# Kernel tuning notes

Measured on AMD Instinct MI355X. Metric: run time of the kernel, lower is better.

## Reference

```python
import jax, jax.numpy as jnp
import numpy as np

N, E = 10000, 160000
IN_C, HID, OUT_C = 128, 128, 64
LAYERS, HEADS = 3, 8
D_HEAD = HID // HEADS


def setup_inputs() -> dict:
    key = jax.random.key(0)
    ks = jax.random.split(key, 12)
    sc = lambda k, shape, fan: (jax.random.normal(k, shape, jnp.float32) / np.float32(np.sqrt(fan)))
    return dict(
        x=jax.random.normal(ks[0], (N, IN_C), jnp.float32),
        edge_index=jax.random.randint(ks[1], (2, E), 0, N, jnp.int32),
        W1=sc(ks[2], (IN_C, HID), IN_C), b1=jnp.zeros((HID,), jnp.float32),
        Wq=sc(ks[3], (LAYERS, HID, HID), HID), bq=jnp.zeros((LAYERS, HID), jnp.float32),
        Wk=sc(ks[4], (LAYERS, HID, HID), HID), bk=jnp.zeros((LAYERS, HID), jnp.float32),
        Wv=sc(ks[5], (LAYERS, HID, HID), HID), bv=jnp.zeros((LAYERS, HID), jnp.float32),
        W2=sc(ks[6], (HID, OUT_C), HID), b2=jnp.zeros((OUT_C,), jnp.float32),
    )


def reference(x, edge_index, W1, b1, Wq, bq, Wk, bk, Wv, bv, W2, b2):
    n = x.shape[0]
    # gcn_norm with self-loops (edge weights = 1)
    loops = jnp.arange(n, dtype=edge_index.dtype)
    src = jnp.concatenate([edge_index[0], loops])  # x_j source nodes
    dst = jnp.concatenate([edge_index[1], loops])  # x_i target nodes (aggregation)
    deg = jax.ops.segment_sum(jnp.ones_like(src, dtype=x.dtype), dst, num_segments=n)
    dinv = jnp.where(deg > 0, jax.lax.rsqrt(deg), jnp.zeros_like(deg))
    norm = dinv[src] * dinv[dst]  # [E+N]

    # dropout layers are identity in eval mode
    h = jax.nn.relu(x @ W1 + b1)
    x_all = h[:, None, :]  # [N, 1, C]

    scale = np.float32(1.0 / np.sqrt(D_HEAD))
    for l in range(LAYERS):
        L = x_all.shape[1]
        # project at node level (linear commutes with gather)
        q = (x_all[:, -1] @ Wq[l] + bq[l])[dst]              # [Et, C], query = last-layer target feats
        k = (x_all @ Wk[l] + bk[l])[src]                     # [Et, L, C], key = source history
        v = (x_all @ Wv[l] + bv[l])[src]                     # [Et, L, C]
        Et = q.shape[0]
        qh = q.reshape(Et, HEADS, D_HEAD)
        kh = k.reshape(Et, L, HEADS, D_HEAD)
        vh = v.reshape(Et, L, HEADS, D_HEAD)
        scores = jnp.einsum('ehd,elhd->ehl', qh, kh) * scale  # attention over history axis L
        attn = jax.nn.softmax(scores, axis=-1)                 # (attn dropout is identity in eval)
        msg = jnp.einsum('ehl,elhd->ehd', attn, vh).reshape(Et, HID)
        agg = jax.ops.segment_sum(norm[:, None] * msg, dst, num_segments=n)
        h_new = jax.nn.relu(agg)
        x_all = jnp.concatenate([x_all, h_new[:, None, :]], axis=1)

    logits = x_all[:, -1] @ W2 + b2
    return jax.nn.log_softmax(logits, axis=1)
```

## Files before the change

kernel.cpp:

```cpp
#include <hip/hip_runtime.h>
#include <hip/hip_fp16.h>
#include <math.h>

#define NN 10000
#define EE 160000
#define HID 128
constexpr int N128 = NN * HID;
constexpr int PSTR = 768;
constexpr int HOFF = 384;

typedef _Float16 f16;
typedef f16 half8 __attribute__((ext_vector_type(8)));
typedef f16 f16x2 __attribute__((ext_vector_type(2)));
typedef float f32x4 __attribute__((ext_vector_type(4)));

#if __has_builtin(__builtin_amdgcn_fdot2)
__device__ inline float fdot2(f16x2 a, f16x2 b, float c) { return __builtin_amdgcn_fdot2(a, b, c, false); }
#else
__device__ inline float fdot2(f16x2 a, f16x2 b, float c) {
    return fmaf((float)a[0], (float)b[0], fmaf((float)a[1], (float)b[1], c));
}
#endif

__global__ __launch_bounds__(256) void cnt_count(const int* __restrict__ dst, int* __restrict__ cnt) {
    int e = blockIdx.x * 256 + threadIdx.x;
    if (e < EE) atomicAdd(&cnt[dst[e]], 1);
}

__global__ __launch_bounds__(256) void scan_rowptr(const int* __restrict__ cnt, int* __restrict__ rowptr,
                                                   float* __restrict__ dinv) {
    __shared__ int part[256];
    const int PER = (NN + 255) / 256;
    int t = threadIdx.x;
    int base = t * PER;
    int sum = 0;
    for (int i = 0; i < PER; ++i) {
        int idx = base + i;
        if (idx < NN) {
            int c = cnt[idx];
            sum += c;
            dinv[idx] = rsqrtf((float)c + 1.0f);
        }
    }
    part[t] = sum;
    __syncthreads();
    for (int ofs = 1; ofs < 256; ofs <<= 1) {
        int v = (t >= ofs) ? part[t - ofs] : 0;
        __syncthreads();
        part[t] += v;
        __syncthreads();
    }
    int run = (t > 0) ? part[t - 1] : 0;
    for (int i = 0; i < PER; ++i) {
        int idx = base + i;
        if (idx <= NN) rowptr[idx] = run;
        if (idx < NN) run += cnt[idx];
    }
}

__global__ __launch_bounds__(256) void scatter_edges(const int* __restrict__ ei,
                                                     const int* __restrict__ rowptr,
                                                     int* __restrict__ fill,
                                                     int* __restrict__ esorted) {
    int e = blockIdx.x * 256 + threadIdx.x;
    if (e < EE) {
        int s = ei[e], d = ei[EE + e];
        int pos = rowptr[d] + atomicAdd(&fill[d], 1);
        esorted[pos] = s;
    }
}

__global__ __launch_bounds__(256) void prep_fused(const float* __restrict__ W1, const float* __restrict__ Wq,
                                                  const float* __restrict__ Wk, const float* __restrict__ Wv,
                                                  const float* __restrict__ W2, f16* __restrict__ Wt,
                                                  int4* __restrict__ zbuf) {
    int b = blockIdx.x;
    int t = threadIdx.x;
    if (b >= 11) {
        zbuf[(b - 11) * 256 + t] = make_int4(0, 0, 0, 0);
        return;
    }
    f16* dst = Wt + (size_t)b * 16384;
    if (b == 10) {
        int oc = t & 63, k0 = (t >> 6) * 32;
        for (int kk = 0; kk < 32; ++kk) {
            int k = k0 + kk;
            dst[oc * 128 + k] = (f16)W2[(size_t)k * 64 + oc];
        }
        return;
    }
    const float* src = (b == 0) ? W1
                     : (b < 4)  ? Wq + (size_t)(b - 1) * 16384
                     : (b < 7)  ? Wk + (size_t)(b - 4) * 16384
                                : Wv + (size_t)(b - 7) * 16384;
    int oc = t >> 1;
    int k0 = (t & 1) * 64;
    for (int kk = 0; kk < 64; ++kk) {
        int k = k0 + kk;
        dst[oc * 128 + k] = (f16)src[k * 128 + oc];
    }
}

struct GJob {
    const void* in; const f16* Wt; const float* bias; const float* rowscale;
    void* out; int ldi; int ldo; int mode; int inF32;
    const f16* Wt2; const float* bias2;
};
struct GJobs { GJob j[7]; };

__global__ __launch_bounds__(256) void gemm_mfma(GJobs jobs, int nrows) {
    const GJob jb = jobs.j[blockIdx.y];
    __shared__ f16 Xl[64 * 128];
    __shared__ f16 Wl[128 * 128];
    const int t = threadIdx.x;
    const int row0 = blockIdx.x * 64;

    half8 zero8;
#pragma unroll
    for (int z = 0; z < 8; ++z) zero8[z] = (f16)0.f;

#pragma unroll
    for (int it = 0; it < 4; ++it) {
        int idx = t + it * 256;
        int r = idx >> 4, c = idx & 15;
        int gr = row0 + r;
        half8 v = zero8;
        if (gr < nrows) {
            if (jb.inF32) {
                const float* fin = (const float*)jb.in + (size_t)gr * jb.ldi + c * 8;
                float4 f0 = ((const float4*)fin)[0];
                float4 f1 = ((const float4*)fin)[1];
                v[0] = (f16)f0.x; v[1] = (f16)f0.y; v[2] = (f16)f0.z; v[3] = (f16)f0.w;
                v[4] = (f16)f1.x; v[5] = (f16)f1.y; v[6] = (f16)f1.z; v[7] = (f16)f1.w;
            } else {
                v = *(const half8*)((const f16*)jb.in + (size_t)gr * jb.ldi + c * 8);
            }
        }
        *(half8*)((char*)Xl + r * 256 + ((c * 16) ^ ((r & 7) << 4))) = v;
    }
#pragma unroll
    for (int it = 0; it < 8; ++it) {
        int idx = t + it * 256;
        int r = idx >> 4, c = idx & 15;
        half8 v = *(const half8*)(jb.Wt + (size_t)r * 128 + c * 8);
        *(half8*)((char*)Wl + r * 256 + ((c * 16) ^ ((r & 7) << 4))) = v;
    }
    __syncthreads();

    const int w = t >> 6, l = t & 63;
    const int lr = l & 15;
    const int lk = l >> 4;

    f32x4 acc[8];
#pragma unroll
    for (int tn = 0; tn < 8; ++tn)
#pragma unroll
        for (int i = 0; i < 4; ++i) acc[tn][i] = 0.f;

    const int arow = w * 16 + lr;
    const int axor = (arow & 7) << 4;
    const int bxor = (lr & 7) << 4;

#pragma unroll
    for (int ks = 0; ks < 4; ++ks) {
        int koff = (ks * 4 + lk) * 16;
        half8 a = *(const half8*)((const char*)Xl + arow * 256 + (koff ^ axor));
#pragma unroll
        for (int tn = 0; tn < 8; ++tn) {
            int oc = tn * 16 + lr;
            half8 b = *(const half8*)((const char*)Wl + oc * 256 + (koff ^ bxor));
            acc[tn] = __builtin_amdgcn_mfma_f32_16x16x32_f16(a, b, acc[tn], 0, 0, 0);
        }
    }

    const int rbase = row0 + w * 16 + (lk << 2);
    float brs[4];
#pragma unroll
    for (int i = 0; i < 4; ++i)
        brs[i] = jb.rowscale ? ((rbase + i < nrows) ? jb.rowscale[rbase + i] : 0.f) : 1.0f;
    float bsv[8];
#pragma unroll
    for (int tn = 0; tn < 8; ++tn) bsv[tn] = jb.bias[tn * 16 + lr];

    if (jb.mode == 0) {
        float* op = (float*)jb.out;
#pragma unroll
        for (int tn = 0; tn < 8; ++tn)
#pragma unroll
            for (int i = 0; i < 4; ++i) {
                int gr = rbase + i;
                if (gr < nrows) op[(size_t)gr * jb.ldo + tn * 16 + lr] = acc[tn][i] + brs[i] * bsv[tn];
            }
    } else if (jb.mode == 1) {
        f16* op = (f16*)jb.out;
#pragma unroll
        for (int tn = 0; tn < 8; ++tn)
#pragma unroll
            for (int i = 0; i < 4; ++i) {
                int gr = rbase + i;
                if (gr < nrows) op[(size_t)gr * jb.ldo + tn * 16 + lr] = (f16)fmaxf(acc[tn][i] + brs[i] * bsv[tn], 0.f);
            }
    } else if (jb.mode == 2) {
        f16* op = (f16*)jb.out;
#pragma unroll
        for (int tn = 0; tn < 8; ++tn)
#pragma unroll
            for (int i = 0; i < 4; ++i) {
                int gr = rbase + i;
                if (gr < nrows) op[(size_t)gr * jb.ldo + tn * 16 + lr] = (f16)(acc[tn][i] + brs[i] * bsv[tn]);
            }
    } else {
        __syncthreads();
#pragma unroll
        for (int tn = 0; tn < 8; ++tn)
#pragma unroll
            for (int i = 0; i < 4; ++i) {
                f16 v = (f16)fmaxf(acc[tn][i] + brs[i] * bsv[tn], 0.f);
                int lrow = w * 16 + (lk << 2) + i;
                int col = tn * 16 + lr;
                int byte = lrow * 256 + ((((col >> 3) * 16) ^ ((lrow & 7) << 4))) + (col & 7) * 2;
                *(f16*)((char*)Xl + byte) = v;
            }
#pragma unroll
        for (int it = 0; it < 4; ++it) {
            int idx = t + it * 256;
            int r = idx >> 4, c = idx & 15;
            half8 v = *(const half8*)(jb.Wt2 + (size_t)r * 128 + c * 8);
            *(half8*)((char*)Wl + r * 256 + ((c * 16) ^ ((r & 7) << 4))) = v;
        }
        __syncthreads();

        f32x4 acc2[4];
#pragma unroll
        for (int tn = 0; tn < 4; ++tn)
#pragma unroll
            for (int i = 0; i < 4; ++i) acc2[tn][i] = 0.f;
#pragma unroll
        for (int ks = 0; ks < 4; ++ks) {
            int koff = (ks * 4 + lk) * 16;
            half8 a = *(const half8*)((const char*)Xl + arow * 256 + (koff ^ axor));
#pragma unroll
            for (int tn = 0; tn < 4; ++tn) {
                int oc = tn * 16 + lr;
                half8 b = *(const half8*)((const char*)Wl + oc * 256 + (koff ^ bxor));
                acc2[tn] = __builtin_amdgcn_mfma_f32_16x16x32_f16(a, b, acc2[tn], 0, 0, 0);
            }
        }
        float bs2[4];
#pragma unroll
        for (int tn = 0; tn < 4; ++tn) bs2[tn] = jb.bias2[tn * 16 + lr];
#pragma unroll
        for (int i = 0; i < 4; ++i) {
            float lg[4];
#pragma unroll
            for (int tn = 0; tn < 4; ++tn) lg[tn] = acc2[tn][i] + bs2[tn];
            float m = fmaxf(fmaxf(lg[0], lg[1]), fmaxf(lg[2], lg[3]));
#pragma unroll
            for (int sft = 1; sft <= 8; sft <<= 1) m = fmaxf(m, __shfl_xor(m, sft));
            float den = 0.f;
#pragma unroll
            for (int tn = 0; tn < 4; ++tn) den += __expf(lg[tn] - m);
#pragma unroll
            for (int sft = 1; sft <= 8; sft <<= 1) den += __shfl_xor(den, sft);
            float lden = logf(den);
            int gr = rbase + i;
            if (gr < nrows) {
                float* op = (float*)jb.out + (size_t)gr * jb.ldo;
#pragma unroll
                for (int tn = 0; tn < 4; ++tn) op[tn * 16 + lr] = lg[tn] - m - lden;
            }
        }
    }
}

__global__ __launch_bounds__(256) void sgather5(
    const int* __restrict__ rowptr, const int* __restrict__ esorted,
    const float* __restrict__ dinv,
    const f16* __restrict__ hsrc , f16* __restrict__ Sh, float* __restrict__ srow) {
    int d = (blockIdx.x * 256 + threadIdx.x) >> 6;
    int lam = threadIdx.x & 63;
    int qe = lam >> 4, le = lam & 15;
    if (d >= NN) return;
    int i0 = rowptr[d], nE = rowptr[d + 1] - i0 + 1;
    float dvd = dinv[d];
    float u[8];
#pragma unroll
    for (int i = 0; i < 8; ++i) u[i] = 0.f;
    float ssum = 0.f;

    auto ldb = [&](int b, float& w, half8& h) {
        int j = b + qe;
        int s = (j < nE - 1) ? esorted[i0 + j] : d;
        w = (j < nE) ? dinv[s] : 0.f;
        h = *(const half8*)(hsrc + (size_t)s * PSTR + le * 8);
    };
    auto cmp = [&](float w, const half8& h) {
#pragma unroll
        for (int i = 0; i < 8; ++i) u[i] = fmaf(w, (float)h[i], u[i]);
        ssum += w;
    };

    float wA, wB; half8 hA, hB;
    ldb(0, wA, hA);
    for (int b = 0; b < nE; b += 8) {
        ldb(b + 4, wB, hB);
        cmp(wA, hA);
        ldb(b + 8, wA, hA);
        cmp(wB, hB);
    }
#pragma unroll
    for (int i = 0; i < 8; ++i) {
        u[i] += __shfl_xor(u[i], 16);
        u[i] += __shfl_xor(u[i], 32);
    }
    ssum += __shfl_xor(ssum, 16);
    ssum += __shfl_xor(ssum, 32);
    if (qe == 0) {
        half8 o;
#pragma unroll
        for (int i = 0; i < 8; ++i) o[i] = (f16)(dvd * u[i]);
        *(half8*)(Sh + (size_t)d * 128 + le * 8) = o;
        if (le == 0) srow[d] = dvd * ssum;
    }
}

template<int L>
__global__ __launch_bounds__(256) void node_attn5(
    const int* __restrict__ rowptr, const int* __restrict__ esorted,
    const float* __restrict__ dinv,
    const f16* __restrict__ qh, const f16* __restrict__ pack,
    f16* __restrict__ uh) {
    int d = (blockIdx.x * 256 + threadIdx.x) >> 6;
    int lam = threadIdx.x & 63;
    int qe = lam >> 4, le = lam & 15;
    if (d >= NN) return;
    int i0 = rowptr[d], nE = rowptr[d + 1] - i0 + 1;
    float dvd = dinv[d];
    half8 q8 = *(const half8*)(qh + (size_t)d * 128 + le * 8);
    const f16x2* qp = (const f16x2*)&q8;
    float u[8];
#pragma unroll
    for (int i = 0; i < 8; ++i) u[i] = 0.f;

    auto ldb = [&](int b, float& w, half8 (&k)[L], half8 (&h)[L]) {
        int j = b + qe;
        int s = (j < nE - 1) ? esorted[i0 + j] : d;
        w = (j < nE) ? dinv[s] : 0.f;
        const f16* bp = pack + (size_t)s * PSTR + le * 8;
#pragma unroll
        for (int l = 0; l < L; ++l) {
            k[l] = *(const half8*)(bp + l * 128);
            h[l] = *(const half8*)(bp + HOFF + l * 128);
        }
    };
    auto cmp = [&](float w, const half8 (&k)[L], const half8 (&h)[L]) {
        float sc[L];
#pragma unroll
        for (int l = 0; l < L; ++l) {
            const f16x2* kp = (const f16x2*)&k[l];
            float p = 0.f;
#pragma unroll
            for (int i = 0; i < 4; ++i) p = fdot2(qp[i], kp[i], p);
            p += __shfl_xor(p, 1);
            sc[l] = p * 0.25f;
        }
        float m = sc[0];
#pragma unroll
        for (int l = 1; l < L; ++l) m = fmaxf(m, sc[l]);
        float den = 0.f;
#pragma unroll
        for (int l = 0; l < L; ++l) { sc[l] = __expf(sc[l] - m); den += sc[l]; }
        float wg = w * __builtin_amdgcn_rcpf(den);
#pragma unroll
        for (int l = 0; l < L; ++l) {
            float a = sc[l] * wg;
#pragma unroll
            for (int i = 0; i < 8; ++i) u[i] = fmaf(a, (float)h[l][i], u[i]);
        }
    };

    float wA, wB; half8 kA[L], hA[L], kB[L], hB[L];
    ldb(0, wA, kA, hA);
    for (int b = 0; b < nE; b += 8) {
        ldb(b + 4, wB, kB, hB);
        cmp(wA, kA, hA);
        ldb(b + 8, wA, kA, hA);
        cmp(wB, kB, hB);
    }
#pragma unroll
    for (int i = 0; i < 8; ++i) {
        u[i] += __shfl_xor(u[i], 16);
        u[i] += __shfl_xor(u[i], 32);
    }
    if (qe == 0) {
        half8 o;
#pragma unroll
        for (int i = 0; i < 8; ++i) o[i] = (f16)(dvd * u[i]);
        *(half8*)(uh + (size_t)d * 128 + le * 8) = o;
    }
}

extern "C" void kernel_launch(void* const* d_in, const int* in_sizes, int n_in,
                              void* d_out, int out_size, void* d_ws, size_t ws_size,
                              hipStream_t stream) {
    (void)in_sizes; (void)n_in; (void)out_size; (void)ws_size;
    const float* x  = (const float*)d_in[0];
    const int*   ei = (const int*)d_in[1];
    const float* W1 = (const float*)d_in[2];
    const float* b1 = (const float*)d_in[3];
    const float* Wq = (const float*)d_in[4];
    const float* bq = (const float*)d_in[5];
    const float* Wk = (const float*)d_in[6];
    const float* bk = (const float*)d_in[7];
    const float* Wv = (const float*)d_in[8];
    const float* bv = (const float*)d_in[9];
    const float* W2 = (const float*)d_in[10];
    const float* b2 = (const float*)d_in[11];
    float* out = (float*)d_out;

    int*    cnt     = (int*)d_ws;
    int*    fill    = cnt + 16384;
    int*    rowptr  = fill + 16384;
    int*    esorted = rowptr + 16384;
    float*  dinv    = (float*)(esorted + 163840);
    float*  srow    = dinv + 16384;
    f16*    pack    = (f16*)(srow + 16384);
    f16*    Sh      = pack + (size_t)NN * PSTR;
    f16*    qh      = Sh + N128;
    f16*    uh      = qh + N128;
    f16*    Wt      = uh + N128;

    prep_fused<<<43, 256, 0, stream>>>(W1, Wq, Wk, Wv, W2, Wt, (int4*)cnt);
    cnt_count<<<(EE + 255) / 256, 256, 0, stream>>>(ei + EE, cnt);
    scan_rowptr<<<1, 256, 0, stream>>>(cnt, rowptr, dinv);
    scatter_edges<<<(EE + 255) / 256, 256, 0, stream>>>(ei, rowptr, fill, esorted);

    const int gx = (NN + 63) / 64;
    auto WT = [&](int m) { return Wt + (size_t)m * 16384; };
    auto H  = [&](int lev) { return pack + HOFF + lev * 128; };
    auto K  = [&](int lev) { return pack + lev * 128; };

    {
        GJobs jobs{};
        jobs.j[0] = {x, WT(0), b1, nullptr, H(0), HID, PSTR, 1, 1, nullptr, nullptr};
        gemm_mfma<<<dim3(gx, 1), 256, 0, stream>>>(jobs, NN);
    }

    const int nblocks = (NN * 64 + 255) / 256;

    sgather5<<<nblocks, 256, 0, stream>>>(rowptr, esorted, dinv, pack + HOFF, Sh, srow);
    {
        GJobs jobs{};
        jobs.j[0] = {Sh, WT(7), bv, srow, H(1), HID, PSTR, 1, 0, nullptr, nullptr};
        gemm_mfma<<<dim3(gx, 1), 256, 0, stream>>>(jobs, NN);
    }

    for (int l = 1; l < 3; ++l) {
        int L = l + 1;
        GJobs jobs{};
        jobs.j[0] = {H(L - 1), WT(1 + l), bq + l * HID, nullptr, qh, PSTR, HID, 2, 0, nullptr, nullptr};
        for (int lev = 0; lev < L; ++lev)
            jobs.j[1 + lev] = {H(lev), WT(4 + l), bk + l * HID, nullptr, K(lev), PSTR, PSTR, 2, 0, nullptr, nullptr};
        gemm_mfma<<<dim3(gx, 1 + L), 256, 0, stream>>>(jobs, NN);

        if (L == 2) node_attn5<2><<<nblocks, 256, 0, stream>>>(rowptr, esorted, dinv, qh, pack, uh);
        if (L == 3) node_attn5<3><<<nblocks, 256, 0, stream>>>(rowptr, esorted, dinv, qh, pack, uh);

        GJobs vjob{};
        if (L == 2) {
            vjob.j[0] = {uh, WT(7 + l), bv + l * HID, srow, H(2), HID, PSTR, 1, 0, nullptr, nullptr};
        } else {
            vjob.j[0] = {uh, WT(7 + l), bv + l * HID, srow, out, HID, 64, 3, 0, WT(10), b2};
        }
        gemm_mfma<<<dim3(gx, 1), 256, 0, stream>>>(vjob, NN);
    }
}
```

Measured before the change: 169.0 us.

## Fold Wq·Wkᵀ per head so attention scores use stored hidden states

```diff
diff --git a/kernel.cpp b/kernel.cpp
--- a/kernel.cpp
+++ b/kernel.cpp
@@ -6,8 +6,7 @@
 #define EE 160000
 #define HID 128
 constexpr int N128 = NN * HID;
-constexpr int PSTR = 768;
-constexpr int HOFF = 384;
+constexpr int PSTR = 384;
 
 typedef _Float16 f16;
 typedef f16 half8 __attribute__((ext_vector_type(8)));
@@ -70,34 +69,61 @@
     }
 }
 
-__global__ __launch_bounds__(256) void prep_fused(const float* __restrict__ W1, const float* __restrict__ Wq,
-                                                  const float* __restrict__ Wk, const float* __restrict__ Wv,
-                                                  const float* __restrict__ W2, f16* __restrict__ Wt,
-                                                  int4* __restrict__ zbuf) {
+__global__ __launch_bounds__(256) void prep_fused(
+    const float* __restrict__ W1, const float* __restrict__ Wq, const float* __restrict__ Wk,
+    const float* __restrict__ Wv, const float* __restrict__ W2, const float* __restrict__ bq,
+    f16* __restrict__ Wt, f16* __restrict__ Wqkt, float* __restrict__ bqk, int4* __restrict__ zbuf) {
+    __shared__ float Wqs[128][16];
+    __shared__ float Wks[128][16];
     int b = blockIdx.x;
     int t = threadIdx.x;
-    if (b >= 11) {
-        zbuf[(b - 11) * 256 + t] = make_int4(0, 0, 0, 0);
+    if (b >= 21) {
+        zbuf[(b - 21) * 256 + t] = make_int4(0, 0, 0, 0);
         return;
     }
-    f16* dst = Wt + (size_t)b * 16384;
-    if (b == 10) {
-        int oc = t & 63, k0 = (t >> 6) * 32;
-        for (int kk = 0; kk < 32; ++kk) {
+    if (b < 5) {
+        f16* dst = Wt + (size_t)b * 16384;
+        if (b == 4) {
+            int oc = t & 63, k0 = (t >> 6) * 32;
+            for (int kk = 0; kk < 32; ++kk) {
+                int k = k0 + kk;
+                dst[oc * 128 + k] = (f16)W2[(size_t)k * 64 + oc];
+            }
+            return;
+        }
+        const float* src = (b == 0) ? W1 : Wv + (size_t)(b - 1) * 16384;
+        int oc = t >> 1;
+        int k0 = (t & 1) * 64;
+        for (int kk = 0; kk < 64; ++kk) {
             int k = k0 + kk;
-            dst[oc * 128 + k] = (f16)W2[(size_t)k * 64 + oc];
+            dst[oc * 128 + k] = (f16)src[k * 128 + oc];
         }
         return;
     }
-    const float* src = (b == 0) ? W1
-                     : (b < 4)  ? Wq + (size_t)(b - 1) * 16384
-                     : (b < 7)  ? Wk + (size_t)(b - 4) * 16384
-                                : Wv + (size_t)(b - 7) * 16384;
-    int oc = t >> 1;
-    int k0 = (t & 1) * 64;
-    for (int kk = 0; kk < 64; ++kk) {
-        int k = k0 + kk;
-        dst[oc * 128 + k] = (f16)src[k * 128 + oc];
+    int idx = b - 5;
+    int l = 1 + (idx >> 3), h = idx & 7;
+    const float* WqL = Wq + (size_t)l * 16384;
+    const float* WkL = Wk + (size_t)l * 16384;
+    for (int i = t; i < 2048; i += 256) {
+        int r = i >> 4, c = i & 15;
+        Wqs[r][c] = WqL[r * 128 + h * 16 + c];
+        Wks[r][c] = WkL[r * 128 + h * 16 + c];
+    }
+    __syncthreads();
+    f16* dst = Wqkt + (size_t)idx * 16384;
+    int j = t >> 1, i0 = (t & 1) * 64;
+    for (int ii = 0; ii < 64; ++ii) {
+        int i = i0 + ii;
+        float s = 0.f;
+#pragma unroll
+        for (int c = 0; c < 16; ++c) s = fmaf(Wqs[i][c], Wks[j][c], s);
+        dst[j * 128 + i] = (f16)s;
+    }
+    if (t < 128) {
+        float s = 0.f;
+#pragma unroll
+        for (int c = 0; c < 16; ++c) s = fmaf(bq[l * 128 + h * 16 + c], Wks[t][c], s);
+        bqk[idx * 128 + t] = s;
     }
 }
 
@@ -106,7 +132,7 @@
     void* out; int ldi; int ldo; int mode; int inF32;
     const f16* Wt2; const float* bias2;
 };
-struct GJobs { GJob j[7]; };
+struct GJobs { GJob j[8]; };
 
 __global__ __launch_bounds__(256) void gemm_mfma(GJobs jobs, int nrows) {
     const GJob jb = jobs.j[blockIdx.y];
@@ -325,10 +351,10 @@
 }
 
 template<int L>
-__global__ __launch_bounds__(256) void node_attn5(
+__global__ __launch_bounds__(256) void node_attn6(
     const int* __restrict__ rowptr, const int* __restrict__ esorted,
     const float* __restrict__ dinv,
-    const f16* __restrict__ qh, const f16* __restrict__ pack,
+    const f16* __restrict__ qkb, const f16* __restrict__ pack,
     f16* __restrict__ uh) {
     int d = (blockIdx.x * 256 + threadIdx.x) >> 6;
     int lam = threadIdx.x & 63;
@@ -336,56 +362,69 @@
     if (d >= NN) return;
     int i0 = rowptr[d], nE = rowptr[d + 1] - i0 + 1;
     float dvd = dinv[d];
-    half8 q8 = *(const half8*)(qh + (size_t)d * 128 + le * 8);
-    const f16x2* qp = (const f16x2*)&q8;
+    half8 qk8[8];
+#pragma unroll
+    for (int hh = 0; hh < 8; ++hh)
+        qk8[hh] = *(const half8*)(qkb + (size_t)d * 1024 + hh * 128 + le * 8);
+    const int g = le >> 1;
+    const bool b2g = g >= 4, b1g = (g & 2) != 0, b0g = (g & 1) != 0;
     float u[8];
 #pragma unroll
     for (int i = 0; i < 8; ++i) u[i] = 0.f;
 
-    auto ldb = [&](int b, float& w, half8 (&k)[L], half8 (&h)[L]) {
+    auto ldb = [&](int b, float& w, half8 (&h)[L]) {
         int j = b + qe;
         int s = (j < nE - 1) ? esorted[i0 + j] : d;
         w = (j < nE) ? dinv[s] : 0.f;
         const f16* bp = pack + (size_t)s * PSTR + le * 8;
 #pragma unroll
+        for (int l = 0; l < L; ++l) h[l] = *(const half8*)(bp + l * 128);
+    };
+    auto cmp = [&](float w, const half8 (&h)[L]) {
+        float sel[L];
+#pragma unroll
         for (int l = 0; l < L; ++l) {
-            k[l] = *(const half8*)(bp + l * 128);
-            h[l] = *(const half8*)(bp + HOFF + l * 128);
+            float ph[8];
+#pragma unroll
+            for (int hh = 0; hh < 8; ++hh) {
+                const f16x2* ap = (const f16x2*)&qk8[hh];
+                const f16x2* hp = (const f16x2*)&h[l];
+                float p = 0.f;
+#pragma unroll
+                for (int i = 0; i < 4; ++i) p = fdot2(ap[i], hp[i], p);
+                ph[hh] = p;
+            }
+#pragma unroll
+            for (int st = 1; st <= 8; st <<= 1) {
+#pragma unroll
+                for (int hh = 0; hh < 8; ++hh) ph[hh] += __shfl_xor(ph[hh], st);
+            }
+            float a = b2g ? (b1g ? (b0g ? ph[7] : ph[6]) : (b0g ? ph[5] : ph[4]))
+                          : (b1g ? (b0g ? ph[3] : ph[2]) : (b0g ? ph[1] : ph[0]));
+            sel[l] = a * 0.25f;
+        }
+        float m = sel[0];
+#pragma unroll
+        for (int l = 1; l < L; ++l) m = fmaxf(m, sel[l]);
+        float den = 0.f;
+#pragma unroll
+        for (int l = 0; l < L; ++l) { sel[l] = __expf(sel[l] - m); den += sel[l]; }
+        float wg = w * __builtin_amdgcn_rcpf(den);
+#pragma unroll
+        for (int l = 0; l < L; ++l) {
+            float a = sel[l] * wg;
+#pragma unroll
+            for (int i = 0; i < 8; ++i) u[i] = fmaf(a, (float)h[l][i], u[i]);
         }
     };
-    auto cmp = [&](float w, const half8 (&k)[L], const half8 (&h)[L]) {
-        float sc[L];
-#pragma unroll
-        for (int l = 0; l < L; ++l) {
-            const f16x2* kp = (const f16x2*)&k[l];
-            float p = 0.f;
-#pragma unroll
-            for (int i = 0; i < 4; ++i) p = fdot2(qp[i], kp[i], p);
-            p += __shfl_xor(p, 1);
-            sc[l] = p * 0.25f;
-        }
-        float m = sc[0];
-#pragma unroll
-        for (int l = 1; l < L; ++l) m = fmaxf(m, sc[l]);
-        float den = 0.f;
-#pragma unroll
-        for (int l = 0; l < L; ++l) { sc[l] = __expf(sc[l] - m); den += sc[l]; }
-        float wg = w * __builtin_amdgcn_rcpf(den);
-#pragma unroll
-        for (int l = 0; l < L; ++l) {
-            float a = sc[l] * wg;
-#pragma unroll
-            for (int i = 0; i < 8; ++i) u[i] = fmaf(a, (float)h[l][i], u[i]);
-        }
-    };
-
-    float wA, wB; half8 kA[L], hA[L], kB[L], hB[L];
-    ldb(0, wA, kA, hA);
+
+    float wA, wB; half8 hA[L], hB[L];
+    ldb(0, wA, hA);
     for (int b = 0; b < nE; b += 8) {
-        ldb(b + 4, wB, kB, hB);
-        cmp(wA, kA, hA);
-        ldb(b + 8, wA, kA, hA);
-        cmp(wB, kB, hB);
+        ldb(b + 4, wB, hB);
+        cmp(wA, hA);
+        ldb(b + 8, wA, hA);
+        cmp(wB, hB);
     }
 #pragma unroll
     for (int i = 0; i < 8; ++i) {
@@ -417,6 +456,7 @@
     const float* W2 = (const float*)d_in[10];
     const float* b2 = (const float*)d_in[11];
     float* out = (float*)d_out;
+    (void)bk;
 
     int*    cnt     = (int*)d_ws;
     int*    fill    = cnt + 16384;
@@ -424,21 +464,22 @@
     int*    esorted = rowptr + 16384;
     float*  dinv    = (float*)(esorted + 163840);
     float*  srow    = dinv + 16384;
-    f16*    pack    = (f16*)(srow + 16384);
+    float*  bqk     = srow + 16384;
+    f16*    pack    = (f16*)(bqk + 2048);
     f16*    Sh      = pack + (size_t)NN * PSTR;
-    f16*    qh      = Sh + N128;
-    f16*    uh      = qh + N128;
-    f16*    Wt      = uh + N128;
-
-    prep_fused<<<43, 256, 0, stream>>>(W1, Wq, Wk, Wv, W2, Wt, (int4*)cnt);
+    f16*    uh      = Sh + N128;
+    f16*    qkbuf   = uh + N128;
+    f16*    Wt      = qkbuf + (size_t)NN * 1024;
+    f16*    Wqkt    = Wt + 5 * 16384;
+
+    prep_fused<<<53, 256, 0, stream>>>(W1, Wq, Wk, Wv, W2, bq, Wt, Wqkt, bqk, (int4*)cnt);
     cnt_count<<<(EE + 255) / 256, 256, 0, stream>>>(ei + EE, cnt);
     scan_rowptr<<<1, 256, 0, stream>>>(cnt, rowptr, dinv);
     scatter_edges<<<(EE + 255) / 256, 256, 0, stream>>>(ei, rowptr, fill, esorted);
 
     const int gx = (NN + 63) / 64;
     auto WT = [&](int m) { return Wt + (size_t)m * 16384; };
-    auto H  = [&](int lev) { return pack + HOFF + lev * 128; };
-    auto K  = [&](int lev) { return pack + lev * 128; };
+    auto H  = [&](int lev) { return pack + lev * 128; };
 
     {
         GJobs jobs{};
@@ -448,29 +489,31 @@
 
     const int nblocks = (NN * 64 + 255) / 256;
 
-    sgather5<<<nblocks, 256, 0, stream>>>(rowptr, esorted, dinv, pack + HOFF, Sh, srow);
+    sgather5<<<nblocks, 256, 0, stream>>>(rowptr, esorted, dinv, pack, Sh, srow);
     {
         GJobs jobs{};
-        jobs.j[0] = {Sh, WT(7), bv, srow, H(1), HID, PSTR, 1, 0, nullptr, nullptr};
+        jobs.j[0] = {Sh, WT(1), bv, srow, H(1), HID, PSTR, 1, 0, nullptr, nullptr};
         gemm_mfma<<<dim3(gx, 1), 256, 0, stream>>>(jobs, NN);
     }
 
     for (int l = 1; l < 3; ++l) {
         int L = l + 1;
         GJobs jobs{};
-        jobs.j[0] = {H(L - 1), WT(1 + l), bq + l * HID, nullptr, qh, PSTR, HID, 2, 0, nullptr, nullptr};
-        for (int lev = 0; lev < L; ++lev)
-            jobs.j[1 + lev] = {H(lev), WT(4 + l), bk + l * HID, nullptr, K(lev), PSTR, PSTR, 2, 0, nullptr, nullptr};
-        gemm_mfma<<<dim3(gx, 1 + L), 256, 0, stream>>>(jobs, NN);
-
-        if (L == 2) node_attn5<2><<<nblocks, 256, 0, stream>>>(rowptr, esorted, dinv, qh, pack, uh);
-        if (L == 3) node_attn5<3><<<nblocks, 256, 0, stream>>>(rowptr, esorted, dinv, qh, pack, uh);
+        for (int h = 0; h < 8; ++h) {
+            int idx = (l - 1) * 8 + h;
+            jobs.j[h] = {H(L - 1), Wqkt + (size_t)idx * 16384, bqk + idx * 128, nullptr,
+                         qkbuf + h * 128, PSTR, 1024, 2, 0, nullptr, nullptr};
+        }
+        gemm_mfma<<<dim3(gx, 8), 256, 0, stream>>>(jobs, NN);
+
+        if (L == 2) node_attn6<2><<<nblocks, 256, 0, stream>>>(rowptr, esorted, dinv, qkbuf, pack, uh);
+        if (L == 3) node_attn6<3><<<nblocks, 256, 0, stream>>>(rowptr, esorted, dinv, qkbuf, pack, uh);
 
         GJobs vjob{};
         if (L == 2) {
-            vjob.j[0] = {uh, WT(7 + l), bv + l * HID, srow, H(2), HID, PSTR, 1, 0, nullptr, nullptr};
+            vjob.j[0] = {uh, WT(2), bv + 128, srow, H(2), HID, PSTR, 1, 0, nullptr, nullptr};
         } else {
-            vjob.j[0] = {uh, WT(7 + l), bv + l * HID, srow, out, HID, 64, 3, 0, WT(10), b2};
+            vjob.j[0] = {uh, WT(3), bv + 256, srow, out, HID, 64, 3, 0, WT(4), b2};
         }
         gemm_mfma<<<dim3(gx, 1), 256, 0, stream>>>(vjob, NN);
     }
```

Measured after the change: 238.9 us. 41.3% more time.

## Split per-node edge aggregation across two wavefronts with partial-sum buffers

Applied to the files above, without the earlier changes.

```diff
diff --git a/kernel.cpp b/kernel.cpp
--- a/kernel.cpp
+++ b/kernel.cpp
@@ -104,7 +104,7 @@
 struct GJob {
     const void* in; const f16* Wt; const float* bias; const float* rowscale;
     void* out; int ldi; int ldo; int mode; int inF32;
-    const f16* Wt2; const float* bias2;
+    const f16* Wt2; const float* bias2; const f16* in2;
 };
 struct GJobs { GJob j[7]; };
 
@@ -134,6 +134,10 @@
                 v[4] = (f16)f1.x; v[5] = (f16)f1.y; v[6] = (f16)f1.z; v[7] = (f16)f1.w;
             } else {
                 v = *(const half8*)((const f16*)jb.in + (size_t)gr * jb.ldi + c * 8);
+                if (jb.in2) {
+                    half8 v2 = *(const half8*)(jb.in2 + (size_t)gr * jb.ldi + c * 8);
+                    v = v + v2;
+                }
             }
         }
         *(half8*)((char*)Xl + r * 256 + ((c * 16) ^ ((r & 7) << 4))) = v;
@@ -273,15 +277,19 @@
     }
 }
 
-__global__ __launch_bounds__(256) void sgather5(
+__global__ __launch_bounds__(256) void sgather6(
     const int* __restrict__ rowptr, const int* __restrict__ esorted,
     const float* __restrict__ dinv,
-    const f16* __restrict__ hsrc , f16* __restrict__ Sh, float* __restrict__ srow) {
-    int d = (blockIdx.x * 256 + threadIdx.x) >> 6;
+    const f16* __restrict__ hsrc , f16* __restrict__ Sh0, f16* __restrict__ Sh1,
+    float* __restrict__ srow) {
+    int wid = (blockIdx.x * 256 + threadIdx.x) >> 6;
     int lam = threadIdx.x & 63;
     int qe = lam >> 4, le = lam & 15;
-    if (d >= NN) return;
+    if (wid >= 2 * NN) return;
+    int d = wid >> 1, half = wid & 1;
     int i0 = rowptr[d], nE = rowptr[d + 1] - i0 + 1;
+    int mid = (nE + 1) >> 1;
+    int lo = half ? mid : 0, hi = half ? nE : mid;
     float dvd = dinv[d];
     float u[8];
 #pragma unroll
@@ -291,7 +299,7 @@
     auto ldb = [&](int b, float& w, half8& h) {
         int j = b + qe;
         int s = (j < nE - 1) ? esorted[i0 + j] : d;
-        w = (j < nE) ? dinv[s] : 0.f;
+        w = (j < hi) ? dinv[s] : 0.f;
         h = *(const half8*)(hsrc + (size_t)s * PSTR + le * 8);
     };
     auto cmp = [&](float w, const half8& h) {
@@ -301,8 +309,8 @@
     };
 
     float wA, wB; half8 hA, hB;
-    ldb(0, wA, hA);
-    for (int b = 0; b < nE; b += 8) {
+    ldb(lo, wA, hA);
+    for (int b = lo; b < hi; b += 8) {
         ldb(b + 4, wB, hB);
         cmp(wA, hA);
         ldb(b + 8, wA, hA);
@@ -316,25 +324,29 @@
     ssum += __shfl_xor(ssum, 16);
     ssum += __shfl_xor(ssum, 32);
     if (qe == 0) {
+        f16* Sh = half ? Sh1 : Sh0;
         half8 o;
 #pragma unroll
         for (int i = 0; i < 8; ++i) o[i] = (f16)(dvd * u[i]);
         *(half8*)(Sh + (size_t)d * 128 + le * 8) = o;
-        if (le == 0) srow[d] = dvd * ssum;
+        if (le == 0) atomicAdd(&srow[d], dvd * ssum);
     }
 }
 
 template<int L>
-__global__ __launch_bounds__(256) void node_attn5(
+__global__ __launch_bounds__(256) void node_attn7(
     const int* __restrict__ rowptr, const int* __restrict__ esorted,
     const float* __restrict__ dinv,
     const f16* __restrict__ qh, const f16* __restrict__ pack,
-    f16* __restrict__ uh) {
-    int d = (blockIdx.x * 256 + threadIdx.x) >> 6;
+    f16* __restrict__ uh0, f16* __restrict__ uh1) {
+    int wid = (blockIdx.x * 256 + threadIdx.x) >> 6;
     int lam = threadIdx.x & 63;
     int qe = lam >> 4, le = lam & 15;
-    if (d >= NN) return;
+    if (wid >= 2 * NN) return;
+    int d = wid >> 1, half = wid & 1;
     int i0 = rowptr[d], nE = rowptr[d + 1] - i0 + 1;
+    int mid = (nE + 1) >> 1;
+    int lo = half ? mid : 0, hi = half ? nE : mid;
     float dvd = dinv[d];
     half8 q8 = *(const half8*)(qh + (size_t)d * 128 + le * 8);
     const f16x2* qp = (const f16x2*)&q8;
@@ -345,7 +357,7 @@
     auto ldb = [&](int b, float& w, half8 (&k)[L], half8 (&h)[L]) {
         int j = b + qe;
         int s = (j < nE - 1) ? esorted[i0 + j] : d;
-        w = (j < nE) ? dinv[s] : 0.f;
+        w = (j < hi) ? dinv[s] : 0.f;
         const f16* bp = pack + (size_t)s * PSTR + le * 8;
 #pragma unroll
         for (int l = 0; l < L; ++l) {
@@ -380,8 +392,8 @@
     };
 
     float wA, wB; half8 kA[L], hA[L], kB[L], hB[L];
-    ldb(0, wA, kA, hA);
-    for (int b = 0; b < nE; b += 8) {
+    ldb(lo, wA, kA, hA);
+    for (int b = lo; b < hi; b += 8) {
         ldb(b + 4, wB, kB, hB);
         cmp(wA, kA, hA);
         ldb(b + 8, wA, kA, hA);
@@ -393,6 +405,7 @@
         u[i] += __shfl_xor(u[i], 32);
     }
     if (qe == 0) {
+        f16* uh = half ? uh1 : uh0;
         half8 o;
 #pragma unroll
         for (int i = 0; i < 8; ++i) o[i] = (f16)(dvd * u[i]);
@@ -420,17 +433,19 @@
 
     int*    cnt     = (int*)d_ws;
     int*    fill    = cnt + 16384;
-    int*    rowptr  = fill + 16384;
+    float*  srow    = (float*)(fill + 16384);
+    int*    rowptr  = (int*)(srow + 16384);
     int*    esorted = rowptr + 16384;
     float*  dinv    = (float*)(esorted + 163840);
-    float*  srow    = dinv + 16384;
-    f16*    pack    = (f16*)(srow + 16384);
-    f16*    Sh      = pack + (size_t)NN * PSTR;
-    f16*    qh      = Sh + N128;
-    f16*    uh      = qh + N128;
-    f16*    Wt      = uh + N128;
-
-    prep_fused<<<43, 256, 0, stream>>>(W1, Wq, Wk, Wv, W2, Wt, (int4*)cnt);
+    f16*    pack    = (f16*)(dinv + 16384);
+    f16*    Sh0     = pack + (size_t)NN * PSTR;
+    f16*    Sh1     = Sh0 + N128;
+    f16*    qh      = Sh1 + N128;
+    f16*    uh0     = qh + N128;
+    f16*    uh1     = uh0 + N128;
+    f16*    Wt      = uh1 + N128;
+
+    prep_fused<<<59, 256, 0, stream>>>(W1, Wq, Wk, Wv, W2, Wt, (int4*)cnt);
     cnt_count<<<(EE + 255) / 256, 256, 0, stream>>>(ei + EE, cnt);
     scan_rowptr<<<1, 256, 0, stream>>>(cnt, rowptr, dinv);
     scatter_edges<<<(EE + 255) / 256, 256, 0, stream>>>(ei, rowptr, fill, esorted);
@@ -442,35 +457,35 @@
 
     {
         GJobs jobs{};
-        jobs.j[0] = {x, WT(0), b1, nullptr, H(0), HID, PSTR, 1, 1, nullptr, nullptr};
+        jobs.j[0] = {x, WT(0), b1, nullptr, H(0), HID, PSTR, 1, 1, nullptr, nullptr, nullptr};
         gemm_mfma<<<dim3(gx, 1), 256, 0, stream>>>(jobs, NN);
     }
 
-    const int nblocks = (NN * 64 + 255) / 256;
-
-    sgather5<<<nblocks, 256, 0, stream>>>(rowptr, esorted, dinv, pack + HOFF, Sh, srow);
+    const int nblocks = (2 * NN * 64 + 255) / 256;
+
+    sgather6<<<nblocks, 256, 0, stream>>>(rowptr, esorted, dinv, pack + HOFF, Sh0, Sh1, srow);
     {
         GJobs jobs{};
-        jobs.j[0] = {Sh, WT(7), bv, srow, H(1), HID, PSTR, 1, 0, nullptr, nullptr};
+        jobs.j[0] = {Sh0, WT(7), bv, srow, H(1), HID, PSTR, 1, 0, nullptr, nullptr, Sh1};
         gemm_mfma<<<dim3(gx, 1), 256, 0, stream>>>(jobs, NN);
     }
 
     for (int l = 1; l < 3; ++l) {
         int L = l + 1;
         GJobs jobs{};
-        jobs.j[0] = {H(L - 1), WT(1 + l), bq + l * HID, nullptr, qh, PSTR, HID, 2, 0, nullptr, nullptr};
+        jobs.j[0] = {H(L - 1), WT(1 + l), bq + l * HID, nullptr, qh, PSTR, HID, 2, 0, nullptr, nullptr, nullptr};
         for (int lev = 0; lev < L; ++lev)
-            jobs.j[1 + lev] = {H(lev), WT(4 + l), bk + l * HID, nullptr, K(lev), PSTR, PSTR, 2, 0, nullptr, nullptr};
+            jobs.j[1 + lev] = {H(lev), WT(4 + l), bk + l * HID, nullptr, K(lev), PSTR, PSTR, 2, 0, nullptr, nullptr, nullptr};
         gemm_mfma<<<dim3(gx, 1 + L), 256, 0, stream>>>(jobs, NN);
 
-        if (L == 2) node_attn5<2><<<nblocks, 256, 0, stream>>>(rowptr, esorted, dinv, qh, pack, uh);
-        if (L == 3) node_attn5<3><<<nblocks, 256, 0, stream>>>(rowptr, esorted, dinv, qh, pack, uh);
+        if (L == 2) node_attn7<2><<<nblocks, 256, 0, stream>>>(rowptr, esorted, dinv, qh, pack, uh0, uh1);
+        if (L == 3) node_attn7<3><<<nblocks, 256, 0, stream>>>(rowptr, esorted, dinv, qh, pack, uh0, uh1);
 
         GJobs vjob{};
         if (L == 2) {
-            vjob.j[0] = {uh, WT(7 + l), bv + l * HID, srow, H(2), HID, PSTR, 1, 0, nullptr, nullptr};
+            vjob.j[0] = {uh0, WT(7 + l), bv + l * HID, srow, H(2), HID, PSTR, 1, 0, nullptr, nullptr, uh1};
         } else {
-            vjob.j[0] = {uh, WT(7 + l), bv + l * HID, srow, out, HID, 64, 3, 0, WT(10), b2};
+            vjob.j[0] = {uh0, WT(7 + l), bv + l * HID, srow, out, HID, 64, 3, 0, WT(10), b2, uh1};
         }
         gemm_mfma<<<dim3(gx, 1), 256, 0, stream>>>(vjob, NN);
     }
```

New measurement: 178.4 us. +5.6%, slower.

## Chain Q/K projections into the producing GEMM epilogue and drop separate projection launches

Applied to the files above, without the earlier changes.

```diff
diff --git a/kernel.cpp b/kernel.cpp
--- a/kernel.cpp
+++ b/kernel.cpp
@@ -6,8 +6,8 @@
 #define EE 160000
 #define HID 128
 constexpr int N128 = NN * HID;
-constexpr int PSTR = 768;
-constexpr int HOFF = 384;
+constexpr int PST = 1024;
+constexpr int H0 = 640;
 
 typedef _Float16 f16;
 typedef f16 half8 __attribute__((ext_vector_type(8)));
@@ -28,7 +28,7 @@
 }
 
 __global__ __launch_bounds__(256) void scan_rowptr(const int* __restrict__ cnt, int* __restrict__ rowptr,
-                                                   float* __restrict__ dinv) {
+                                                   int* __restrict__ rowfill, float* __restrict__ dinv) {
     __shared__ int part[256];
     const int PER = (NN + 255) / 256;
     int t = threadIdx.x;
@@ -54,18 +54,17 @@
     for (int i = 0; i < PER; ++i) {
         int idx = base + i;
         if (idx <= NN) rowptr[idx] = run;
-        if (idx < NN) run += cnt[idx];
+        if (idx < NN) { rowfill[idx] = run; run += cnt[idx]; }
     }
 }
 
 __global__ __launch_bounds__(256) void scatter_edges(const int* __restrict__ ei,
-                                                     const int* __restrict__ rowptr,
-                                                     int* __restrict__ fill,
+                                                     int* __restrict__ rowfill,
                                                      int* __restrict__ esorted) {
     int e = blockIdx.x * 256 + threadIdx.x;
     if (e < EE) {
         int s = ei[e], d = ei[EE + e];
-        int pos = rowptr[d] + atomicAdd(&fill[d], 1);
+        int pos = atomicAdd(&rowfill[d], 1);
         esorted[pos] = s;
     }
 }
@@ -76,12 +75,12 @@
                                                   int4* __restrict__ zbuf) {
     int b = blockIdx.x;
     int t = threadIdx.x;
-    if (b >= 11) {
-        zbuf[(b - 11) * 256 + t] = make_int4(0, 0, 0, 0);
+    if (b >= 9) {
+        zbuf[(b - 9) * 256 + t] = make_int4(0, 0, 0, 0);
         return;
     }
     f16* dst = Wt + (size_t)b * 16384;
-    if (b == 10) {
+    if (b == 4) {
         int oc = t & 63, k0 = (t >> 6) * 32;
         for (int kk = 0; kk < 32; ++kk) {
             int k = k0 + kk;
@@ -90,9 +89,11 @@
         return;
     }
     const float* src = (b == 0) ? W1
-                     : (b < 4)  ? Wq + (size_t)(b - 1) * 16384
-                     : (b < 7)  ? Wk + (size_t)(b - 4) * 16384
-                                : Wv + (size_t)(b - 7) * 16384;
+                     : (b <= 3) ? Wv + (size_t)(b - 1) * 16384
+                     : (b == 5) ? Wq + 16384
+                     : (b == 6) ? Wq + 2 * 16384
+                     : (b == 7) ? Wk + 16384
+                                : Wk + 2 * 16384;
     int oc = t >> 1;
     int k0 = (t & 1) * 64;
     for (int kk = 0; kk < 64; ++kk) {
@@ -101,15 +102,16 @@
     }
 }
 
-struct GJob {
-    const void* in; const f16* Wt; const float* bias; const float* rowscale;
-    void* out; int ldi; int ldo; int mode; int inF32;
-    const f16* Wt2; const float* bias2;
+struct Proj { const f16* Wt; const float* bias; f16* out; int ldo; };
+struct FJob {
+    const void* in; int inF32; int ldi;
+    const f16* Wt; const float* bias; const float* rowscale;
+    f16* out; int ldo; int writeOut;
+    int nproj; Proj proj[3];
+    int doFinal; const f16* Wt2; const float* bias2; float* fout;
 };
-struct GJobs { GJob j[7]; };
-
-__global__ __launch_bounds__(256) void gemm_mfma(GJobs jobs, int nrows) {
-    const GJob jb = jobs.j[blockIdx.y];
+
+__global__ __launch_bounds__(256) void gemm_fused(FJob jb, int nrows) {
     __shared__ f16 Xl[64 * 128];
     __shared__ f16 Wl[128 * 128];
     const int t = threadIdx.x;
@@ -150,16 +152,15 @@
     const int w = t >> 6, l = t & 63;
     const int lr = l & 15;
     const int lk = l >> 4;
-
-    f32x4 acc[8];
-#pragma unroll
-    for (int tn = 0; tn < 8; ++tn)
-#pragma unroll
-        for (int i = 0; i < 4; ++i) acc[tn][i] = 0.f;
-
     const int arow = w * 16 + lr;
     const int axor = (arow & 7) << 4;
     const int bxor = (lr & 7) << 4;
+
+    f32x4 acc[8];
+#pragma unroll
+    for (int tn = 0; tn < 8; ++tn)
+#pragma unroll
+        for (int i = 0; i < 4; ++i) acc[tn][i] = 0.f;
 
 #pragma unroll
     for (int ks = 0; ks < 4; ++ks) {
@@ -182,45 +183,60 @@
 #pragma unroll
     for (int tn = 0; tn < 8; ++tn) bsv[tn] = jb.bias[tn * 16 + lr];
 
-    if (jb.mode == 0) {
-        float* op = (float*)jb.out;
+#pragma unroll
+    for (int tn = 0; tn < 8; ++tn)
+#pragma unroll
+        for (int i = 0; i < 4; ++i) {
+            f16 v = (f16)fmaxf(acc[tn][i] + brs[i] * bsv[tn], 0.f);
+            int lrow = w * 16 + (lk << 2) + i;
+            int col = tn * 16 + lr;
+            int byte = lrow * 256 + (((col >> 3) * 16) ^ ((lrow & 7) << 4)) + (col & 7) * 2;
+            *(f16*)((char*)Xl + byte) = v;
+            int gr = rbase + i;
+            if (jb.writeOut && gr < nrows) jb.out[(size_t)gr * jb.ldo + col] = v;
+        }
+
+    for (int p = 0; p < jb.nproj; ++p) {
+        Proj pr = jb.proj[p];
+        __syncthreads();
+#pragma unroll
+        for (int it = 0; it < 8; ++it) {
+            int idx = t + it * 256;
+            int r = idx >> 4, c = idx & 15;
+            half8 v = *(const half8*)(pr.Wt + (size_t)r * 128 + c * 8);
+            *(half8*)((char*)Wl + r * 256 + ((c * 16) ^ ((r & 7) << 4))) = v;
+        }
+        __syncthreads();
+
+#pragma unroll
+        for (int tn = 0; tn < 8; ++tn)
+#pragma unroll
+            for (int i = 0; i < 4; ++i) acc[tn][i] = 0.f;
+#pragma unroll
+        for (int ks = 0; ks < 4; ++ks) {
+            int koff = (ks * 4 + lk) * 16;
+            half8 a = *(const half8*)((const char*)Xl + arow * 256 + (koff ^ axor));
+#pragma unroll
+            for (int tn = 0; tn < 8; ++tn) {
+                int oc = tn * 16 + lr;
+                half8 b = *(const half8*)((const char*)Wl + oc * 256 + (koff ^ bxor));
+                acc[tn] = __builtin_amdgcn_mfma_f32_16x16x32_f16(a, b, acc[tn], 0, 0, 0);
+            }
+        }
+        float bp[8];
+#pragma unroll
+        for (int tn = 0; tn < 8; ++tn) bp[tn] = pr.bias[tn * 16 + lr];
 #pragma unroll
         for (int tn = 0; tn < 8; ++tn)
 #pragma unroll
             for (int i = 0; i < 4; ++i) {
                 int gr = rbase + i;
-                if (gr < nrows) op[(size_t)gr * jb.ldo + tn * 16 + lr] = acc[tn][i] + brs[i] * bsv[tn];
+                if (gr < nrows) pr.out[(size_t)gr * pr.ldo + tn * 16 + lr] = (f16)(acc[tn][i] + bp[tn]);
             }
-    } else if (jb.mode == 1) {
-        f16* op = (f16*)jb.out;
-#pragma unroll
-        for (int tn = 0; tn < 8; ++tn)
-#pragma unroll
-            for (int i = 0; i < 4; ++i) {
-                int gr = rbase + i;
-                if (gr < nrows) op[(size_t)gr * jb.ldo + tn * 16 + lr] = (f16)fmaxf(acc[tn][i] + brs[i] * bsv[tn], 0.f);
-            }
-    } else if (jb.mode == 2) {
-        f16* op = (f16*)jb.out;
-#pragma unroll
-        for (int tn = 0; tn < 8; ++tn)
-#pragma unroll
-            for (int i = 0; i < 4; ++i) {
-                int gr = rbase + i;
-                if (gr < nrows) op[(size_t)gr * jb.ldo + tn * 16 + lr] = (f16)(acc[tn][i] + brs[i] * bsv[tn]);
-            }
-    } else {
+    }
+
+    if (jb.doFinal) {
         __syncthreads();
-#pragma unroll
-        for (int tn = 0; tn < 8; ++tn)
-#pragma unroll
-            for (int i = 0; i < 4; ++i) {
-                f16 v = (f16)fmaxf(acc[tn][i] + brs[i] * bsv[tn], 0.f);
-                int lrow = w * 16 + (lk << 2) + i;
-                int col = tn * 16 + lr;
-                int byte = lrow * 256 + ((((col >> 3) * 16) ^ ((lrow & 7) << 4))) + (col & 7) * 2;
-                *(f16*)((char*)Xl + byte) = v;
-            }
 #pragma unroll
         for (int it = 0; it < 4; ++it) {
             int idx = t + it * 256;
@@ -265,7 +281,7 @@
             float lden = logf(den);
             int gr = rbase + i;
             if (gr < nrows) {
-                float* op = (float*)jb.out + (size_t)gr * jb.ldo;
+                float* op = jb.fout + (size_t)gr * 64;
 #pragma unroll
                 for (int tn = 0; tn < 4; ++tn) op[tn * 16 + lr] = lg[tn] - m - lden;
             }
@@ -276,7 +292,7 @@
 __global__ __launch_bounds__(256) void sgather5(
     const int* __restrict__ rowptr, const int* __restrict__ esorted,
     const float* __restrict__ dinv,
-    const f16* __restrict__ hsrc , f16* __restrict__ Sh, float* __restrict__ srow) {
+    const f16* __restrict__ pack, f16* __restrict__ Sh, float* __restrict__ srow) {
     int d = (blockIdx.x * 256 + threadIdx.x) >> 6;
     int lam = threadIdx.x & 63;
     int qe = lam >> 4, le = lam & 15;
@@ -292,7 +308,7 @@
         int j = b + qe;
         int s = (j < nE - 1) ? esorted[i0 + j] : d;
         w = (j < nE) ? dinv[s] : 0.f;
-        h = *(const half8*)(hsrc + (size_t)s * PSTR + le * 8);
+        h = *(const half8*)(pack + (size_t)s * PST + H0 + le * 8);
     };
     auto cmp = [&](float w, const half8& h) {
 #pragma unroll
@@ -324,8 +340,8 @@
     }
 }
 
-template<int L>
-__global__ __launch_bounds__(256) void node_attn5(
+template<int L, int KOFF>
+__global__ __launch_bounds__(256) void node_attn8(
     const int* __restrict__ rowptr, const int* __restrict__ esorted,
     const float* __restrict__ dinv,
     const f16* __restrict__ qh, const f16* __restrict__ pack,
@@ -346,11 +362,11 @@
         int j = b + qe;
         int s = (j < nE - 1) ? esorted[i0 + j] : d;
         w = (j < nE) ? dinv[s] : 0.f;
-        const f16* bp = pack + (size_t)s * PSTR + le * 8;
+        const f16* bp = pack + (size_t)s * PST + le * 8;
 #pragma unroll
         for (int l = 0; l < L; ++l) {
-            k[l] = *(const half8*)(bp + l * 128);
-            h[l] = *(const half8*)(bp + HOFF + l * 128);
+            k[l] = *(const half8*)(bp + KOFF + l * 128);
+            h[l] = *(const half8*)(bp + H0 + l * 128);
         }
     };
     auto cmp = [&](float w, const half8 (&k)[L], const half8 (&h)[L]) {
@@ -419,59 +435,74 @@
     float* out = (float*)d_out;
 
     int*    cnt     = (int*)d_ws;
-    int*    fill    = cnt + 16384;
-    int*    rowptr  = fill + 16384;
+    int*    rowfill = cnt + 16384;
+    int*    rowptr  = rowfill + 16384;
     int*    esorted = rowptr + 16384;
     float*  dinv    = (float*)(esorted + 163840);
     float*  srow    = dinv + 16384;
     f16*    pack    = (f16*)(srow + 16384);
-    f16*    Sh      = pack + (size_t)NN * PSTR;
+    f16*    Sh      = pack + (size_t)NN * PST;
     f16*    qh      = Sh + N128;
     f16*    uh      = qh + N128;
     f16*    Wt      = uh + N128;
 
-    prep_fused<<<43, 256, 0, stream>>>(W1, Wq, Wk, Wv, W2, Wt, (int4*)cnt);
+    auto WT = [&](int m) { return Wt + (size_t)m * 16384; };
+
+    prep_fused<<<25, 256, 0, stream>>>(W1, Wq, Wk, Wv, W2, Wt, (int4*)cnt);
     cnt_count<<<(EE + 255) / 256, 256, 0, stream>>>(ei + EE, cnt);
-    scan_rowptr<<<1, 256, 0, stream>>>(cnt, rowptr, dinv);
-    scatter_edges<<<(EE + 255) / 256, 256, 0, stream>>>(ei, rowptr, fill, esorted);
+    scan_rowptr<<<1, 256, 0, stream>>>(cnt, rowptr, rowfill, dinv);
+    scatter_edges<<<(EE + 255) / 256, 256, 0, stream>>>(ei, rowfill, esorted);
 
     const int gx = (NN + 63) / 64;
-    auto WT = [&](int m) { return Wt + (size_t)m * 16384; };
-    auto H  = [&](int lev) { return pack + HOFF + lev * 128; };
-    auto K  = [&](int lev) { return pack + lev * 128; };
+    const int nblocks = (NN * 64 + 255) / 256;
 
     {
-        GJobs jobs{};
-        jobs.j[0] = {x, WT(0), b1, nullptr, H(0), HID, PSTR, 1, 1, nullptr, nullptr};
-        gemm_mfma<<<dim3(gx, 1), 256, 0, stream>>>(jobs, NN);
-    }
-
-    const int nblocks = (NN * 64 + 255) / 256;
-
-    sgather5<<<nblocks, 256, 0, stream>>>(rowptr, esorted, dinv, pack + HOFF, Sh, srow);
+        FJob j{};
+        j.in = x; j.inF32 = 1; j.ldi = HID;
+        j.Wt = WT(0); j.bias = b1; j.rowscale = nullptr;
+        j.out = pack + H0; j.ldo = PST; j.writeOut = 1;
+        j.nproj = 2;
+        j.proj[0] = {WT(7), bk + HID,     pack + 0,   PST};
+        j.proj[1] = {WT(8), bk + 2 * HID, pack + 256, PST};
+        gemm_fused<<<gx, 256, 0, stream>>>(j, NN);
+    }
+
+    sgather5<<<nblocks, 256, 0, stream>>>(rowptr, esorted, dinv, pack, Sh, srow);
+
     {
-        GJobs jobs{};
-        jobs.j[0] = {Sh, WT(7), bv, srow, H(1), HID, PSTR, 1, 0, nullptr, nullptr};
-        gemm_mfma<<<dim3(gx, 1), 256, 0, stream>>>(jobs, NN);
-    }
-
-    for (int l = 1; l < 3; ++l) {
-        int L = l + 1;
-        GJobs jobs{};
-        jobs.j[0] = {H(L - 1), WT(1 + l), bq + l * HID, nullptr, qh, PSTR, HID, 2, 0, nullptr, nullptr};
-        for (int lev = 0; lev < L; ++lev)
-            jobs.j[1 + lev] = {H(lev), WT(4 + l), bk + l * HID, nullptr, K(lev), PSTR, PSTR, 2, 0, nullptr, nullptr};
-        gemm_mfma<<<dim3(gx, 1 + L), 256, 0, stream>>>(jobs, NN);
-
-        if (L == 2) node_attn5<2><<<nblocks, 256, 0, stream>>>(rowptr, esorted, dinv, qh, pack, uh);
-        if (L == 3) node_attn5<3><<<nblocks, 256, 0, stream>>>(rowptr, esorted, dinv, qh, pack, uh);
-
-        GJobs vjob{};
-        if (L == 2) {
-            vjob.j[0] = {uh, WT(7 + l), bv + l * HID, srow, H(2), HID, PSTR, 1, 0, nullptr, nullptr};
-        } else {
-            vjob.j[0] = {uh, WT(7 + l), bv + l * HID, srow, out, HID, 64, 3, 0, WT(10), b2};
-        }
-        gemm_mfma<<<dim3(gx, 1), 256, 0, stream>>>(vjob, NN);
-    }
-}
+        FJob j{};
+        j.in = Sh; j.inF32 = 0; j.ldi = HID;
+        j.Wt = WT(1); j.bias = bv; j.rowscale = srow;
+        j.out = pack + H0 + 128; j.ldo = PST; j.writeOut = 1;
+        j.nproj = 3;
+        j.proj[0] = {WT(5), bq + HID,     qh,         HID};
+        j.proj[1] = {WT(7), bk + HID,     pack + 128, PST};
+        j.proj[2] = {WT(8), bk + 2 * HID, pack + 384, PST};
+        gemm_fused<<<gx, 256, 0, stream>>>(j, NN);
+    }
+
+    node_attn8<2, 0><<<nblocks, 256, 0, stream>>>(rowptr, esorted, dinv, qh, pack, uh);
+
+    {
+        FJob j{};
+        j.in = uh; j.inF32 = 0; j.ldi = HID;
+        j.Wt = WT(2); j.bias = bv + HID; j.rowscale = srow;
+        j.out = pack + H0 + 256; j.ldo = PST; j.writeOut = 1;
+        j.nproj = 2;
+        j.proj[0] = {WT(6), bq + 2 * HID, qh,         HID};
+        j.proj[1] = {WT(8), bk + 2 * HID, pack + 512, PST};
+        gemm_fused<<<gx, 256, 0, stream>>>(j, NN);
+    }
+
+    node_attn8<3, 256><<<nblocks, 256, 0, stream>>>(rowptr, esorted, dinv, qh, pack, uh);
+
+    {
+        FJob j{};
+        j.in = uh; j.inF32 = 0; j.ldi = HID;
+        j.Wt = WT(3); j.bias = bv + 2 * HID; j.rowscale = srow;
+        j.out = nullptr; j.ldo = HID; j.writeOut = 0;
+        j.nproj = 0;
+        j.doFinal = 1; j.Wt2 = WT(4); j.bias2 = b2; j.fout = out;
+        gemm_fused<<<gx, 256, 0, stream>>>(j, NN);
+    }
+}
```

Result: slower. 180.0 us (+6.5%).
